# Kernel optimization log

Hardware: AMD Instinct MI355X
Metric: run time of the kernel (lower is better)

Reference implementation:

```python
import jax, jax.numpy as jnp
import numpy as np

N = 50000      # nodes
E = 800000     # edges (avg degree 16)
F_IN = 3       # dataset.num_node_features
H = 256        # hidden_channels
G = 64         # batch_size (num graphs)
OUT = 24       # lin_out output dim


def setup_inputs() -> dict:
    key = jax.random.key(0)
    ks = jax.random.split(key, 16)
    s = 0.05
    inp = {
        "x": jax.random.normal(ks[0], (N, F_IN), jnp.float32),
        "edge_index": jax.random.randint(ks[1], (2, E), 0, N, dtype=jnp.int32),
        "batch": jnp.sort(jax.random.randint(ks[2], (N,), 0, G, dtype=jnp.int32)),
        # layer 1 (F_IN -> H)
        "w_rel1": jax.random.normal(ks[3], (F_IN, H), jnp.float32) * s,
        "w_root1": jax.random.normal(ks[4], (F_IN, H), jnp.float32) * s,
        "b1": jnp.zeros((H,), jnp.float32),
        # layers 2..7 (H -> H), stacked
        "w_rel": jax.random.normal(ks[5], (6, H, H), jnp.float32) * s,
        "w_root": jax.random.normal(ks[6], (6, H, H), jnp.float32) * s,
        "b": jnp.zeros((6, H), jnp.float32),
        # output head
        "w_out": jax.random.normal(ks[7], (H, OUT), jnp.float32) * s,
        "b_out": jnp.zeros((OUT,), jnp.float32),
    }
    return inp


def reference(x, edge_index, batch, w_rel1, w_root1, b1, w_rel, w_root, b, w_out, b_out):
    src, dst = edge_index[0], edge_index[1]

    def conv(h, wr, wro, bb):
        # PyG GraphConv with add aggregation:
        # out_i = W_rel @ sum_{j -> i} h_j + b + W_root @ h_i
        agg = jax.ops.segment_sum(h[src], dst, num_segments=N)
        return agg @ wr + h @ wro + bb

    h = jax.nn.relu(conv(x, w_rel1, w_root1, b1))
    for i in range(6):
        h = jax.nn.relu(conv(h, w_rel[i], w_root[i], b[i]))

    # global_mean_pool over batch segment ids
    counts = jax.ops.segment_sum(jnp.ones((N,), h.dtype), batch, num_segments=G)
    pooled = jax.ops.segment_sum(h, batch, num_segments=G) / jnp.maximum(counts, 1.0)[:, None]

    # dropout is identity in eval mode
    return pooled @ w_out + b_out
```

## Files before the change

### kernel.cpp

```cpp
#include <hip/hip_runtime.h>

#define N_NODES 50000
#define MPAD 50048
#define N_EDGES 800000
#define H 256
#define K_CAT 512
#define G_BATCH 64
#define OUT_DIM 24

#define SCAN_BLK 256
#define NBLK ((N_NODES + SCAN_BLK - 1) / SCAN_BLK)

typedef __attribute__((ext_vector_type(8))) short short8;
typedef __attribute__((ext_vector_type(4))) float float4v;

__device__ __forceinline__ float bf2f(unsigned short u) {
    return __uint_as_float(((unsigned)u) << 16);
}
__device__ __forceinline__ unsigned short f2bf(float f) {
    unsigned x = __float_as_uint(f);
    unsigned r = (x + 0x7FFFu + ((x >> 16) & 1u)) >> 16;
    return (unsigned short)r;
}

__device__ __forceinline__ void async_copy16(void* lds, const void* g) {
    __builtin_amdgcn_global_load_lds(
        (const __attribute__((address_space(1))) unsigned int*)g,
        (__attribute__((address_space(3))) unsigned int*)lds, 16, 0, 0);
}



__global__ void histo_kernel(const int* __restrict__ dst, int* __restrict__ deg,
                             int* __restrict__ epos) {
    int e = blockIdx.x * blockDim.x + threadIdx.x;
    if (e < N_EDGES) epos[e] = atomicAdd(&deg[dst[e]], 1);
}

__global__ void scan_block(const int* __restrict__ deg, int* __restrict__ rowptr,
                           int* __restrict__ blockSums) {
    __shared__ int s[SCAN_BLK];
    int idx = blockIdx.x * SCAN_BLK + threadIdx.x;
    int v = (idx < N_NODES) ? deg[idx] : 0;
    s[threadIdx.x] = v;
    __syncthreads();
    for (int off = 1; off < SCAN_BLK; off <<= 1) {
        int t = (threadIdx.x >= off) ? s[threadIdx.x - off] : 0;
        __syncthreads();
        s[threadIdx.x] += t;
        __syncthreads();
    }
    if (idx < N_NODES) rowptr[idx] = s[threadIdx.x] - v;
    if (threadIdx.x == SCAN_BLK - 1) blockSums[blockIdx.x] = s[threadIdx.x];
}

__global__ void scan_finish(int* __restrict__ rowptr, const int* __restrict__ blockSums) {
    __shared__ int s[SCAN_BLK];
    int t = threadIdx.x;
    int v = (t < NBLK) ? blockSums[t] : 0;
    s[t] = v;
    __syncthreads();
    for (int off = 1; off < SCAN_BLK; off <<= 1) {
        int tv = (t >= off) ? s[t - off] : 0;
        __syncthreads();
        s[t] += tv;
        __syncthreads();
    }
    int prefix = (blockIdx.x > 0) ? s[blockIdx.x - 1] : 0;
    int idx = blockIdx.x * SCAN_BLK + t;
    if (idx < N_NODES) rowptr[idx] += prefix;
    if (blockIdx.x == 0 && t == 0) rowptr[N_NODES] = s[NBLK - 1];
}

__global__ void fill_csr(const int* __restrict__ src, const int* __restrict__ dst,
                         const int* __restrict__ rowptr, const int* __restrict__ epos,
                         int* __restrict__ csr_src) {
    int e = blockIdx.x * blockDim.x + threadIdx.x;
    if (e >= N_EDGES) return;
    csr_src[rowptr[dst[e]] + epos[e]] = src[e];
}


__global__ void prep_weights(const float* __restrict__ w_rel, const float* __restrict__ w_root,
                             unsigned short* __restrict__ WcatT) {
    int idx = blockIdx.x * blockDim.x + threadIdx.x;
    if (idx >= 6 * K_CAT * H) return;
    int n = idx & (H - 1);
    int k = (idx >> 8) & (K_CAT - 1);
    int l = idx >> 17;
    float v;
    if (k < H) {
        int f = (k & 0xC0) | ((k & 3) << 4) | ((k >> 2) & 15);
        v = w_rel[(size_t)l * H * H + f * H + n];
    } else {
        v = w_root[(size_t)l * H * H + (k - H) * H + n];
    }
    WcatT[(size_t)l * H * K_CAT + (size_t)n * K_CAT + k] = f2bf(v);
}


__global__ void agg3(const float* __restrict__ x, const int* __restrict__ rowptr,
                     const int* __restrict__ csr_src, float* __restrict__ agg) {
    int n = blockIdx.x * blockDim.x + threadIdx.x;
    if (n >= N_NODES) return;
    int beg = rowptr[n], end = rowptr[n + 1];
    float a0 = 0.f, a1 = 0.f, a2 = 0.f;
    for (int i = beg; i < end; ++i) {
        int s = csr_src[i];
        a0 += x[s * 3 + 0];
        a1 += x[s * 3 + 1];
        a2 += x[s * 3 + 2];
    }
    agg[n * 3 + 0] = a0;
    agg[n * 3 + 1] = a1;
    agg[n * 3 + 2] = a2;
}

__global__ void layer1_kernel(const float* __restrict__ x, const float* __restrict__ agg,
                              const float* __restrict__ wr, const float* __restrict__ wro,
                              const float* __restrict__ bias, unsigned short* __restrict__ cat,
                              unsigned char* __restrict__ h8, float* __restrict__ hscale) {
    __shared__ unsigned char tmp[H];
    int n = blockIdx.x;
    int f = threadIdx.x;
    float a0 = agg[n * 3 + 0], a1 = agg[n * 3 + 1], a2 = agg[n * 3 + 2];
    float x0 = x[n * 3 + 0], x1 = x[n * 3 + 1], x2 = x[n * 3 + 2];
    float v = bias[f];
    v += a0 * wr[0 * H + f] + a1 * wr[1 * H + f] + a2 * wr[2 * H + f];
    v += x0 * wro[0 * H + f] + x1 * wro[1 * H + f] + x2 * wro[2 * H + f];
    v = fmaxf(v, 0.f);
    cat[(size_t)n * K_CAT + H + f] = f2bf(v);
    float m = v;
#pragma unroll
    for (int off = 1; off < 64; off <<= 1) m = fmaxf(m, __shfl_xor(m, off, 64));
    float inv = m > 0.f ? 255.f / m : 0.f;
    tmp[(f & 0xC0) | ((f & 15) << 2) | ((f >> 4) & 3)] = (unsigned char)(v * inv + 0.5f);
    if ((f & 63) == 0) hscale[n * 4 + (f >> 6)] = m * (1.f / 255.f);
    __syncthreads();
    if (f < 64) *(unsigned*)(h8 + (size_t)n * H + f * 4) = *(const unsigned*)(tmp + f * 4);
}


__global__ __launch_bounds__(256) void aggH(unsigned short* __restrict__ cat,
                                            const unsigned char* __restrict__ h8,
                                            const float* __restrict__ hscale,
                                            const int* __restrict__ rowptr,
                                            const int* __restrict__ csr_src) {
    int gtid = blockIdx.x * blockDim.x + threadIdx.x;
    int node = gtid >> 6;
    if (node >= N_NODES) return;
    int lane = threadIdx.x & 63;
    int sub = lane >> 4;
    int fl = lane & 15;
    int g = fl >> 2;
    int beg = rowptr[node], end = rowptr[node + 1];

    if (beg >= end) {
        if (sub == 0) {
            uint4 z = make_uint4(0, 0, 0, 0);
            unsigned short* o = cat + (size_t)node * K_CAT + fl * 16;
            *(uint4*)o = z;
            *(uint4*)(o + 8) = z;
        }
        return;
    }

    float acc[16] = {};
    const unsigned char* base = h8 + fl * 16;
    int last = end - 1;

    int ia = beg + sub;
    int ca = ia < end ? ia : last;
    int sa = csr_src[ca];
    int ib = beg + 4 + sub;
    int cb = ib < end ? ib : last;
    int sb = csr_src[cb];
    float sca = (ia < end) ? hscale[sa * 4 + g] : 0.f;
    uint4 qa = *(const uint4*)(base + (size_t)sa * H);

    for (int i = beg; i < end; i += 4) {
        int ic = i + 8 + sub;
        int cc = ic < end ? ic : last;
        int sn = csr_src[cc];
        int inb = i + 4 + sub;
        float scb = (inb < end) ? hscale[sb * 4 + g] : 0.f;
        uint4 qb = *(const uint4*)(base + (size_t)sb * H);

        float sc = sca;
        acc[0]  = fmaf((float)(qa.x & 0xffu), sc, acc[0]);
        acc[1]  = fmaf((float)((qa.x >> 8) & 0xffu), sc, acc[1]);
        acc[2]  = fmaf((float)((qa.x >> 16) & 0xffu), sc, acc[2]);
        acc[3]  = fmaf((float)(qa.x >> 24), sc, acc[3]);
        acc[4]  = fmaf((float)(qa.y & 0xffu), sc, acc[4]);
        acc[5]  = fmaf((float)((qa.y >> 8) & 0xffu), sc, acc[5]);
        acc[6]  = fmaf((float)((qa.y >> 16) & 0xffu), sc, acc[6]);
        acc[7]  = fmaf((float)(qa.y >> 24), sc, acc[7]);
        acc[8]  = fmaf((float)(qa.z & 0xffu), sc, acc[8]);
        acc[9]  = fmaf((float)((qa.z >> 8) & 0xffu), sc, acc[9]);
        acc[10] = fmaf((float)((qa.z >> 16) & 0xffu), sc, acc[10]);
        acc[11] = fmaf((float)(qa.z >> 24), sc, acc[11]);
        acc[12] = fmaf((float)(qa.w & 0xffu), sc, acc[12]);
        acc[13] = fmaf((float)((qa.w >> 8) & 0xffu), sc, acc[13]);
        acc[14] = fmaf((float)((qa.w >> 16) & 0xffu), sc, acc[14]);
        acc[15] = fmaf((float)(qa.w >> 24), sc, acc[15]);

        sa = sb; sb = sn; sca = scb; qa = qb;
    }

#pragma unroll
    for (int j = 0; j < 16; j++) {
        acc[j] += __shfl_xor(acc[j], 16, 64);
        acc[j] += __shfl_xor(acc[j], 32, 64);
    }

    if (sub == 0) {
        unsigned short* o = cat + (size_t)node * K_CAT + fl * 16;
        uint4 p0, p1;
        p0.x = (unsigned)f2bf(acc[0])  | ((unsigned)f2bf(acc[1]) << 16);
        p0.y = (unsigned)f2bf(acc[2])  | ((unsigned)f2bf(acc[3]) << 16);
        p0.z = (unsigned)f2bf(acc[4])  | ((unsigned)f2bf(acc[5]) << 16);
        p0.w = (unsigned)f2bf(acc[6])  | ((unsigned)f2bf(acc[7]) << 16);
        p1.x = (unsigned)f2bf(acc[8])  | ((unsigned)f2bf(acc[9]) << 16);
        p1.y = (unsigned)f2bf(acc[10]) | ((unsigned)f2bf(acc[11]) << 16);
        p1.z = (unsigned)f2bf(acc[12]) | ((unsigned)f2bf(acc[13]) << 16);
        p1.w = (unsigned)f2bf(acc[14]) | ((unsigned)f2bf(acc[15]) << 16);
        *(uint4*)o = p0;
        *(uint4*)(o + 8) = p1;
    }
}


#define GBM 128
#define GBN 128
#define GBK 64

__global__ __launch_bounds__(256) void gemm_mfma(
    const unsigned short* __restrict__ cat, const unsigned short* __restrict__ WcatT,
    const float* __restrict__ bias, unsigned short* __restrict__ catOut,
    unsigned char* __restrict__ h8, float* __restrict__ hscale) {
    __shared__ unsigned short sA[GBM][GBK];
    __shared__ unsigned short sB[GBN][GBK];

    const int tid = threadIdx.x;
    const int wave = tid >> 6;
    const int lane = tid & 63;
    const int quad = lane >> 4;
    const int l16 = lane & 15;
    const int wm0 = (wave & 1) * 64;
    const int wn0 = (wave >> 1) * 64;
    const int m0 = blockIdx.x * GBM;
    const int n0 = blockIdx.y * GBN;

    const int rowoff = lane >> 3;
    const int schunk = ((lane & 7) ^ rowoff) * 8;
    const unsigned short* Asrc[4];
    const unsigned short* Bsrc[4];
#pragma unroll
    for (int j = 0; j < 4; j++) {
        int q = wave * 4 + j;
        Asrc[j] = cat + (size_t)(m0 + q * 8 + rowoff) * K_CAT + schunk;
        Bsrc[j] = WcatT + (size_t)(n0 + q * 8 + rowoff) * K_CAT + schunk;
    }

    const int sw = l16 & 7;
    const int ca0 = (quad ^ sw) * 8;
    const int ca1 = ((4 + quad) ^ sw) * 8;

    float4v acc[4][4] = {};

    for (int kk = 0; kk < K_CAT; kk += GBK) {
#pragma unroll
        for (int j = 0; j < 4; j++) {
            char* da = (char*)sA + (wave * 4 + j) * 1024;
            char* db = (char*)sB + (wave * 4 + j) * 1024;
            async_copy16(da, Asrc[j] + kk);
            async_copy16(db, Bsrc[j] + kk);
        }
        __syncthreads();

        short8 a[4][2], b[4][2];
#pragma unroll
        for (int i = 0; i < 4; i++) {
            const unsigned short* ra = &sA[wm0 + i * 16 + l16][0];
            const unsigned short* rb = &sB[wn0 + i * 16 + l16][0];
            a[i][0] = *(const short8*)(ra + ca0);
            a[i][1] = *(const short8*)(ra + ca1);
            b[i][0] = *(const short8*)(rb + ca0);
            b[i][1] = *(const short8*)(rb + ca1);
        }
#pragma unroll
        for (int sub = 0; sub < 2; sub++)
#pragma unroll
            for (int mi = 0; mi < 4; mi++)
#pragma unroll
                for (int ni = 0; ni < 4; ni++)
                    acc[mi][ni] = __builtin_amdgcn_mfma_f32_16x16x32_bf16(
                        a[mi][sub], b[ni][sub], acc[mi][ni], 0, 0, 0);
        __syncthreads();
    }

    const int hb = n0 + wn0 + l16 * 4;
    const int gsc = (n0 + wn0) >> 6;
    float bcol[4];
#pragma unroll
    for (int ni = 0; ni < 4; ni++) bcol[ni] = bias[n0 + wn0 + ni * 16 + l16];

#pragma unroll
    for (int mi = 0; mi < 4; mi++) {
        int rowb = m0 + wm0 + mi * 16 + quad * 4;
#pragma unroll
        for (int r = 0; r < 4; r++) {
            int row = rowb + r;
            float v0 = fmaxf(acc[mi][0][r] + bcol[0], 0.f);
            float v1 = fmaxf(acc[mi][1][r] + bcol[1], 0.f);
            float v2 = fmaxf(acc[mi][2][r] + bcol[2], 0.f);
            float v3 = fmaxf(acc[mi][3][r] + bcol[3], 0.f);
            unsigned short* co = catOut + (size_t)row * K_CAT + H + n0 + wn0 + l16;
            co[0]  = f2bf(v0);
            co[16] = f2bf(v1);
            co[32] = f2bf(v2);
            co[48] = f2bf(v3);
            float m = fmaxf(fmaxf(v0, v1), fmaxf(v2, v3));
            m = fmaxf(m, __shfl_xor(m, 1, 64));
            m = fmaxf(m, __shfl_xor(m, 2, 64));
            m = fmaxf(m, __shfl_xor(m, 4, 64));
            m = fmaxf(m, __shfl_xor(m, 8, 64));
            float inv = m > 0.f ? 255.f / m : 0.f;
            unsigned p = (unsigned)(v0 * inv + 0.5f)
                       | ((unsigned)(v1 * inv + 0.5f) << 8)
                       | ((unsigned)(v2 * inv + 0.5f) << 16)
                       | ((unsigned)(v3 * inv + 0.5f) << 24);
            *(unsigned*)(h8 + (size_t)row * H + hb) = p;
            if (l16 == 0) hscale[row * 4 + gsc] = m * (1.f / 255.f);
        }
    }
}


__device__ __forceinline__ int lowerBound(const int* __restrict__ batch, int val) {
    int lo = 0, hi = N_NODES;
    while (lo < hi) {
        int mid = (lo + hi) >> 1;
        if (batch[mid] < val) lo = mid + 1; else hi = mid;
    }
    return lo;
}

__global__ void pool_partial(const unsigned short* __restrict__ cat, const int* __restrict__ batch,
                             float* __restrict__ pooled) {
    int g = blockIdx.x;
    int seg = blockIdx.y;
    int f = threadIdx.x;
    int start = lowerBound(batch, g);
    int end = lowerBound(batch, g + 1);
    int len = end - start;
    int s0 = start + (int)((long long)len * seg / 8);
    int s1 = start + (int)((long long)len * (seg + 1) / 8);
    float sum = 0.f;
    for (int n = s0; n < s1; ++n)
        sum += bf2f(cat[(size_t)n * K_CAT + H + f]);
    if (s1 > s0)
        atomicAdd(&pooled[g * H + f], sum);
}

__global__ void head_kernel(const float* __restrict__ pooled, const int* __restrict__ batch,
                            const float* __restrict__ w_out, const float* __restrict__ b_out,
                            float* __restrict__ out) {
    int g = blockIdx.x;
    int o = threadIdx.x;
    int start = lowerBound(batch, g);
    int end = lowerBound(batch, g + 1);
    float cnt = fmaxf((float)(end - start), 1.f);
    float sum = 0.f;
    for (int f = 0; f < H; ++f)
        sum += pooled[g * H + f] * w_out[f * OUT_DIM + o];
    out[g * OUT_DIM + o] = b_out[o] + sum / cnt;
}


extern "C" void kernel_launch(void* const* d_in, const int* in_sizes, int n_in,
                              void* d_out, int out_size, void* d_ws, size_t ws_size,
                              hipStream_t stream) {
    const float* x      = (const float*)d_in[0];
    const int*   ei     = (const int*)d_in[1];
    const int*   batch  = (const int*)d_in[2];
    const float* w_rel1 = (const float*)d_in[3];
    const float* w_root1= (const float*)d_in[4];
    const float* b1     = (const float*)d_in[5];
    const float* w_rel  = (const float*)d_in[6];
    const float* w_root = (const float*)d_in[7];
    const float* b      = (const float*)d_in[8];
    const float* w_out  = (const float*)d_in[9];
    const float* b_out  = (const float*)d_in[10];
    float* out = (float*)d_out;

    const int* src = ei;
    const int* dst = ei + N_EDGES;

    unsigned short* catA  = (unsigned short*)d_ws;
    unsigned short* catB  = catA + (size_t)MPAD * K_CAT;
    unsigned short* WcatT = catB + (size_t)MPAD * K_CAT;
    float* agg3buf = (float*)(WcatT + (size_t)6 * H * K_CAT);
    float* pooled  = agg3buf + (size_t)N_NODES * 4;
    float* hscale  = pooled + G_BATCH * H;
    int* rowptr    = (int*)(hscale + (size_t)MPAD * 4);
    int* degcur    = rowptr + (N_NODES + 1);
    int* blockSums = degcur + N_NODES;
    int* csr_src   = blockSums + SCAN_BLK;
    int* epos      = csr_src + N_EDGES;
    unsigned char* h8 = (unsigned char*)(epos + N_EDGES);

    hipMemsetAsync(degcur, 0, N_NODES * sizeof(int), stream);
    histo_kernel<<<(N_EDGES + 255) / 256, 256, 0, stream>>>(dst, degcur, epos);
    scan_block<<<NBLK, SCAN_BLK, 0, stream>>>(degcur, rowptr, blockSums);
    scan_finish<<<NBLK, SCAN_BLK, 0, stream>>>(rowptr, blockSums);
    fill_csr<<<(N_EDGES + 255) / 256, 256, 0, stream>>>(src, dst, rowptr, epos, csr_src);

    prep_weights<<<(6 * K_CAT * H + 255) / 256, 256, 0, stream>>>(w_rel, w_root, WcatT);

    agg3<<<(N_NODES + 255) / 256, 256, 0, stream>>>(x, rowptr, csr_src, agg3buf);
    layer1_kernel<<<N_NODES, H, 0, stream>>>(x, agg3buf, w_rel1, w_root1, b1, catA, h8, hscale);

    unsigned short* cur = catA;
    unsigned short* nxt = catB;
    for (int l = 0; l < 6; ++l) {
        aggH<<<(N_NODES * 64 + 255) / 256, 256, 0, stream>>>(cur, h8, hscale, rowptr, csr_src);
        dim3 grid(MPAD / GBM, H / GBN);
        gemm_mfma<<<grid, 256, 0, stream>>>(cur, WcatT + (size_t)l * H * K_CAT,
                                            b + (size_t)l * H, nxt, h8, hscale);
        unsigned short* t = cur; cur = nxt; nxt = t;
    }

    hipMemsetAsync(pooled, 0, G_BATCH * H * sizeof(float), stream);
    pool_partial<<<dim3(G_BATCH, 8), 256, 0, stream>>>(cur, batch, pooled);
    head_kernel<<<G_BATCH, OUT_DIM, 0, stream>>>(pooled, batch, w_out, b_out, out);
}
```

Measured before the change: 680.0 us.

## Switch u8 quantization to per-column scales and aggregate with packed integer adds

Replaces per-node, per-64-group u8 scales with per-feature-column max scales. The column maxima are gathered with atomicMax in the GEMM epilogue, and a separate quant_u8 pass writes h8. Because the scale no longer varies per node, aggH can sum raw u8 bytes with packed SIMD integer adds into 16-bit lanes and apply the scale once at the end. This removes the per-edge scale load and the float FMAs. It adds an extra quantize pass per layer, a colmax pass after layer 1, and a permuted feature layout applied to the weights and the head. A per-column scale may lose precision for nodes whose values are much smaller than the column maximum.

```diff
diff --git a/kernel.cpp b/kernel.cpp
--- a/kernel.cpp
+++ b/kernel.cpp
@@ -14,21 +14,21 @@
 typedef __attribute__((ext_vector_type(8))) short short8;
 typedef __attribute__((ext_vector_type(4))) float float4v;
 
-__device__ __forceinline__ float bf2f(unsigned short u) {
-    return __uint_as_float(((unsigned)u) << 16);
-}
+
 __device__ __forceinline__ unsigned short f2bf(float f) {
     unsigned x = __float_as_uint(f);
     unsigned r = (x + 0x7FFFu + ((x >> 16) & 1u)) >> 16;
     return (unsigned short)r;
 }
+__device__ __forceinline__ float bf2f(unsigned short u) {
+    return __uint_as_float(((unsigned)u) << 16);
+}
 
 __device__ __forceinline__ void async_copy16(void* lds, const void* g) {
     __builtin_amdgcn_global_load_lds(
         (const __attribute__((address_space(1))) unsigned int*)g,
         (__attribute__((address_space(3))) unsigned int*)lds, 16, 0, 0);
 }
-
 
 
 __global__ void histo_kernel(const int* __restrict__ dst, int* __restrict__ deg,
@@ -93,7 +93,9 @@
         int f = (k & 0xC0) | ((k & 3) << 4) | ((k >> 2) & 15);
         v = w_rel[(size_t)l * H * H + f * H + n];
     } else {
-        v = w_root[(size_t)l * H * H + (k - H) * H + n];
+        int kk = k - H;
+        int f = (kk & 0xC0) | ((kk & 3) << 4) | ((kk >> 2) & 15);
+        v = w_root[(size_t)l * H * H + f * H + n];
     }
     WcatT[(size_t)l * H * K_CAT + (size_t)n * K_CAT + k] = f2bf(v);
 }
@@ -118,9 +120,7 @@
 
 __global__ void layer1_kernel(const float* __restrict__ x, const float* __restrict__ agg,
                               const float* __restrict__ wr, const float* __restrict__ wro,
-                              const float* __restrict__ bias, unsigned short* __restrict__ cat,
-                              unsigned char* __restrict__ h8, float* __restrict__ hscale) {
-    __shared__ unsigned char tmp[H];
+                              const float* __restrict__ bias, unsigned short* __restrict__ cat) {
     int n = blockIdx.x;
     int f = threadIdx.x;
     float a0 = agg[n * 3 + 0], a1 = agg[n * 3 + 1], a2 = agg[n * 3 + 2];
@@ -128,22 +128,57 @@
     float v = bias[f];
     v += a0 * wr[0 * H + f] + a1 * wr[1 * H + f] + a2 * wr[2 * H + f];
     v += x0 * wro[0 * H + f] + x1 * wro[1 * H + f] + x2 * wro[2 * H + f];
-    v = fmaxf(v, 0.f);
-    cat[(size_t)n * K_CAT + H + f] = f2bf(v);
-    float m = v;
-#pragma unroll
-    for (int off = 1; off < 64; off <<= 1) m = fmaxf(m, __shfl_xor(m, off, 64));
-    float inv = m > 0.f ? 255.f / m : 0.f;
-    tmp[(f & 0xC0) | ((f & 15) << 2) | ((f >> 4) & 3)] = (unsigned char)(v * inv + 0.5f);
-    if ((f & 63) == 0) hscale[n * 4 + (f >> 6)] = m * (1.f / 255.f);
+    int bpos = (f & 0xC0) | ((f & 15) << 2) | ((f >> 4) & 3);
+    cat[(size_t)n * K_CAT + H + bpos] = f2bf(fmaxf(v, 0.f));
+}
+
+
+__global__ __launch_bounds__(256) void colmax_h(const unsigned short* __restrict__ cat,
+                                                float* __restrict__ cs) {
+    int wave = threadIdx.x >> 6, lane = threadIdx.x & 63;
+    int r0 = blockIdx.x * 512 + wave * 128;
+    float m0 = 0.f, m1 = 0.f, m2 = 0.f, m3 = 0.f;
+    for (int i = 0; i < 128; i++) {
+        int r = r0 + i;
+        if (r >= N_NODES) break;
+        uint2 v = *(const uint2*)(cat + (size_t)r * K_CAT + H + lane * 4);
+        m0 = fmaxf(m0, __uint_as_float(v.x << 16));
+        m1 = fmaxf(m1, __uint_as_float(v.x & 0xffff0000u));
+        m2 = fmaxf(m2, __uint_as_float(v.y << 16));
+        m3 = fmaxf(m3, __uint_as_float(v.y & 0xffff0000u));
+    }
+    atomicMax((unsigned*)&cs[lane * 4 + 0], __float_as_uint(m0));
+    atomicMax((unsigned*)&cs[lane * 4 + 1], __float_as_uint(m1));
+    atomicMax((unsigned*)&cs[lane * 4 + 2], __float_as_uint(m2));
+    atomicMax((unsigned*)&cs[lane * 4 + 3], __float_as_uint(m3));
+}
+
+
+__global__ __launch_bounds__(256) void quant_u8(const unsigned short* __restrict__ cat,
+                                                const float* __restrict__ cs,
+                                                unsigned char* __restrict__ h8) {
+    __shared__ float inv[H];
+    int t = threadIdx.x;
+    float c = cs[t];
+    inv[t] = c > 0.f ? 255.f / c : 0.f;
     __syncthreads();
-    if (f < 64) *(unsigned*)(h8 + (size_t)n * H + f * 4) = *(const unsigned*)(tmp + f * 4);
+    int node = blockIdx.x * 4 + (t >> 6);
+    if (node >= N_NODES) return;
+    int s4 = (t & 63) * 4;
+    uint2 v = *(const uint2*)(cat + (size_t)node * K_CAT + H + s4);
+    float f0 = __uint_as_float(v.x << 16), f1 = __uint_as_float(v.x & 0xffff0000u);
+    float f2 = __uint_as_float(v.y << 16), f3 = __uint_as_float(v.y & 0xffff0000u);
+    unsigned q = (unsigned)(f0 * inv[s4] + 0.5f)
+               | ((unsigned)(f1 * inv[s4 + 1] + 0.5f) << 8)
+               | ((unsigned)(f2 * inv[s4 + 2] + 0.5f) << 16)
+               | ((unsigned)(f3 * inv[s4 + 3] + 0.5f) << 24);
+    *(unsigned*)(h8 + (size_t)node * H + s4) = q;
 }
 
 
 __global__ __launch_bounds__(256) void aggH(unsigned short* __restrict__ cat,
                                             const unsigned char* __restrict__ h8,
-                                            const float* __restrict__ hscale,
+                                            const float* __restrict__ cs,
                                             const int* __restrict__ rowptr,
                                             const int* __restrict__ csr_src) {
     int gtid = blockIdx.x * blockDim.x + threadIdx.x;
@@ -152,81 +187,75 @@
     int lane = threadIdx.x & 63;
     int sub = lane >> 4;
     int fl = lane & 15;
-    int g = fl >> 2;
     int beg = rowptr[node], end = rowptr[node + 1];
+    unsigned short* o = cat + (size_t)node * K_CAT + fl * 16;
 
     if (beg >= end) {
         if (sub == 0) {
             uint4 z = make_uint4(0, 0, 0, 0);
-            unsigned short* o = cat + (size_t)node * K_CAT + fl * 16;
             *(uint4*)o = z;
             *(uint4*)(o + 8) = z;
         }
         return;
     }
 
-    float acc[16] = {};
+    unsigned accE[4] = {0, 0, 0, 0}, accO[4] = {0, 0, 0, 0};
     const unsigned char* base = h8 + fl * 16;
     int last = end - 1;
 
-    int ia = beg + sub;
-    int ca = ia < end ? ia : last;
-    int sa = csr_src[ca];
-    int ib = beg + 4 + sub;
-    int cb = ib < end ? ib : last;
-    int sb = csr_src[cb];
-    float sca = (ia < end) ? hscale[sa * 4 + g] : 0.f;
-    uint4 qa = *(const uint4*)(base + (size_t)sa * H);
-
-    for (int i = beg; i < end; i += 4) {
-        int ic = i + 8 + sub;
-        int cc = ic < end ? ic : last;
-        int sn = csr_src[cc];
-        int inb = i + 4 + sub;
-        float scb = (inb < end) ? hscale[sb * 4 + g] : 0.f;
-        uint4 qb = *(const uint4*)(base + (size_t)sb * H);
-
-        float sc = sca;
-        acc[0]  = fmaf((float)(qa.x & 0xffu), sc, acc[0]);
-        acc[1]  = fmaf((float)((qa.x >> 8) & 0xffu), sc, acc[1]);
-        acc[2]  = fmaf((float)((qa.x >> 16) & 0xffu), sc, acc[2]);
-        acc[3]  = fmaf((float)(qa.x >> 24), sc, acc[3]);
-        acc[4]  = fmaf((float)(qa.y & 0xffu), sc, acc[4]);
-        acc[5]  = fmaf((float)((qa.y >> 8) & 0xffu), sc, acc[5]);
-        acc[6]  = fmaf((float)((qa.y >> 16) & 0xffu), sc, acc[6]);
-        acc[7]  = fmaf((float)(qa.y >> 24), sc, acc[7]);
-        acc[8]  = fmaf((float)(qa.z & 0xffu), sc, acc[8]);
-        acc[9]  = fmaf((float)((qa.z >> 8) & 0xffu), sc, acc[9]);
-        acc[10] = fmaf((float)((qa.z >> 16) & 0xffu), sc, acc[10]);
-        acc[11] = fmaf((float)(qa.z >> 24), sc, acc[11]);
-        acc[12] = fmaf((float)(qa.w & 0xffu), sc, acc[12]);
-        acc[13] = fmaf((float)((qa.w >> 8) & 0xffu), sc, acc[13]);
-        acc[14] = fmaf((float)((qa.w >> 16) & 0xffu), sc, acc[14]);
-        acc[15] = fmaf((float)(qa.w >> 24), sc, acc[15]);
-
-        sa = sb; sb = sn; sca = scb; qa = qb;
-    }
-
-#pragma unroll
-    for (int j = 0; j < 16; j++) {
-        acc[j] += __shfl_xor(acc[j], 16, 64);
-        acc[j] += __shfl_xor(acc[j], 32, 64);
-    }
-
-    if (sub == 0) {
-        unsigned short* o = cat + (size_t)node * K_CAT + fl * 16;
-        uint4 p0, p1;
-        p0.x = (unsigned)f2bf(acc[0])  | ((unsigned)f2bf(acc[1]) << 16);
-        p0.y = (unsigned)f2bf(acc[2])  | ((unsigned)f2bf(acc[3]) << 16);
-        p0.z = (unsigned)f2bf(acc[4])  | ((unsigned)f2bf(acc[5]) << 16);
-        p0.w = (unsigned)f2bf(acc[6])  | ((unsigned)f2bf(acc[7]) << 16);
-        p1.x = (unsigned)f2bf(acc[8])  | ((unsigned)f2bf(acc[9]) << 16);
-        p1.y = (unsigned)f2bf(acc[10]) | ((unsigned)f2bf(acc[11]) << 16);
-        p1.z = (unsigned)f2bf(acc[12]) | ((unsigned)f2bf(acc[13]) << 16);
-        p1.w = (unsigned)f2bf(acc[14]) | ((unsigned)f2bf(acc[15]) << 16);
-        *(uint4*)o = p0;
-        *(uint4*)(o + 8) = p1;
-    }
+    for (int i0 = beg; i0 < end; i0 += 4) {
+        int idx = i0 + sub;
+        int s = csr_src[idx < end ? idx : last];
+        uint4 q = *(const uint4*)(base + (size_t)s * H);
+        if (idx >= end) { q.x = 0u; q.y = 0u; q.z = 0u; q.w = 0u; }
+        accE[0] += q.x & 0x00FF00FFu;  accO[0] += (q.x >> 8) & 0x00FF00FFu;
+        accE[1] += q.y & 0x00FF00FFu;  accO[1] += (q.y >> 8) & 0x00FF00FFu;
+        accE[2] += q.z & 0x00FF00FFu;  accO[2] += (q.z >> 8) & 0x00FF00FFu;
+        accE[3] += q.w & 0x00FF00FFu;  accO[3] += (q.w >> 8) & 0x00FF00FFu;
+    }
+
+#pragma unroll
+    for (int j = 0; j < 4; j++) {
+        accE[j] += __shfl_xor(accE[j], 16, 64);
+        accE[j] += __shfl_xor(accE[j], 32, 64);
+        accO[j] += __shfl_xor(accO[j], 16, 64);
+        accO[j] += __shfl_xor(accO[j], 32, 64);
+    }
+    if (sub != 0) return;
+
+    const float k = 1.f / 255.f;
+    float4 c0 = *(const float4*)(cs + fl * 16);
+    float4 c1 = *(const float4*)(cs + fl * 16 + 4);
+    float4 c2 = *(const float4*)(cs + fl * 16 + 8);
+    float4 c3 = *(const float4*)(cs + fl * 16 + 12);
+    float v0  = (float)(accE[0] & 0xFFFFu) * (c0.x * k);
+    float v1  = (float)(accO[0] & 0xFFFFu) * (c0.y * k);
+    float v2  = (float)(accE[0] >> 16)     * (c0.z * k);
+    float v3  = (float)(accO[0] >> 16)     * (c0.w * k);
+    float v4  = (float)(accE[1] & 0xFFFFu) * (c1.x * k);
+    float v5  = (float)(accO[1] & 0xFFFFu) * (c1.y * k);
+    float v6  = (float)(accE[1] >> 16)     * (c1.z * k);
+    float v7  = (float)(accO[1] >> 16)     * (c1.w * k);
+    float v8  = (float)(accE[2] & 0xFFFFu) * (c2.x * k);
+    float v9  = (float)(accO[2] & 0xFFFFu) * (c2.y * k);
+    float v10 = (float)(accE[2] >> 16)     * (c2.z * k);
+    float v11 = (float)(accO[2] >> 16)     * (c2.w * k);
+    float v12 = (float)(accE[3] & 0xFFFFu) * (c3.x * k);
+    float v13 = (float)(accO[3] & 0xFFFFu) * (c3.y * k);
+    float v14 = (float)(accE[3] >> 16)     * (c3.z * k);
+    float v15 = (float)(accO[3] >> 16)     * (c3.w * k);
+
+    uint4 p0, p1;
+    p0.x = (unsigned)f2bf(v0)  | ((unsigned)f2bf(v1) << 16);
+    p0.y = (unsigned)f2bf(v2)  | ((unsigned)f2bf(v3) << 16);
+    p0.z = (unsigned)f2bf(v4)  | ((unsigned)f2bf(v5) << 16);
+    p0.w = (unsigned)f2bf(v6)  | ((unsigned)f2bf(v7) << 16);
+    p1.x = (unsigned)f2bf(v8)  | ((unsigned)f2bf(v9) << 16);
+    p1.y = (unsigned)f2bf(v10) | ((unsigned)f2bf(v11) << 16);
+    p1.z = (unsigned)f2bf(v12) | ((unsigned)f2bf(v13) << 16);
+    p1.w = (unsigned)f2bf(v14) | ((unsigned)f2bf(v15) << 16);
+    *(uint4*)o = p0;
+    *(uint4*)(o + 8) = p1;
 }
 
 
@@ -237,7 +266,7 @@
 __global__ __launch_bounds__(256) void gemm_mfma(
     const unsigned short* __restrict__ cat, const unsigned short* __restrict__ WcatT,
     const float* __restrict__ bias, unsigned short* __restrict__ catOut,
-    unsigned char* __restrict__ h8, float* __restrict__ hscale) {
+    float* __restrict__ csNext) {
     __shared__ unsigned short sA[GBM][GBK];
     __shared__ unsigned short sB[GBN][GBK];
 
@@ -299,11 +328,11 @@
         __syncthreads();
     }
 
-    const int hb = n0 + wn0 + l16 * 4;
-    const int gsc = (n0 + wn0) >> 6;
+    const int colbase = n0 + wn0;
     float bcol[4];
 #pragma unroll
-    for (int ni = 0; ni < 4; ni++) bcol[ni] = bias[n0 + wn0 + ni * 16 + l16];
+    for (int ni = 0; ni < 4; ni++) bcol[ni] = bias[colbase + ni * 16 + l16];
+    float cm[4] = {0.f, 0.f, 0.f, 0.f};
 
 #pragma unroll
     for (int mi = 0; mi < 4; mi++) {
@@ -315,24 +344,26 @@
             float v1 = fmaxf(acc[mi][1][r] + bcol[1], 0.f);
             float v2 = fmaxf(acc[mi][2][r] + bcol[2], 0.f);
             float v3 = fmaxf(acc[mi][3][r] + bcol[3], 0.f);
-            unsigned short* co = catOut + (size_t)row * K_CAT + H + n0 + wn0 + l16;
-            co[0]  = f2bf(v0);
-            co[16] = f2bf(v1);
-            co[32] = f2bf(v2);
-            co[48] = f2bf(v3);
-            float m = fmaxf(fmaxf(v0, v1), fmaxf(v2, v3));
-            m = fmaxf(m, __shfl_xor(m, 1, 64));
-            m = fmaxf(m, __shfl_xor(m, 2, 64));
-            m = fmaxf(m, __shfl_xor(m, 4, 64));
-            m = fmaxf(m, __shfl_xor(m, 8, 64));
-            float inv = m > 0.f ? 255.f / m : 0.f;
-            unsigned p = (unsigned)(v0 * inv + 0.5f)
-                       | ((unsigned)(v1 * inv + 0.5f) << 8)
-                       | ((unsigned)(v2 * inv + 0.5f) << 16)
-                       | ((unsigned)(v3 * inv + 0.5f) << 24);
-            *(unsigned*)(h8 + (size_t)row * H + hb) = p;
-            if (l16 == 0) hscale[row * 4 + gsc] = m * (1.f / 255.f);
+            uint2 p;
+            p.x = (unsigned)f2bf(v0) | ((unsigned)f2bf(v1) << 16);
+            p.y = (unsigned)f2bf(v2) | ((unsigned)f2bf(v3) << 16);
+            *(uint2*)(catOut + (size_t)row * K_CAT + H + colbase + l16 * 4) = p;
+            bool val = row < N_NODES;
+            cm[0] = fmaxf(cm[0], val ? v0 : 0.f);
+            cm[1] = fmaxf(cm[1], val ? v1 : 0.f);
+            cm[2] = fmaxf(cm[2], val ? v2 : 0.f);
+            cm[3] = fmaxf(cm[3], val ? v3 : 0.f);
         }
+    }
+#pragma unroll
+    for (int ni = 0; ni < 4; ni++) {
+        cm[ni] = fmaxf(cm[ni], __shfl_xor(cm[ni], 16, 64));
+        cm[ni] = fmaxf(cm[ni], __shfl_xor(cm[ni], 32, 64));
+    }
+    if (quad == 0) {
+#pragma unroll
+        for (int ni = 0; ni < 4; ni++)
+            atomicMax((unsigned*)&csNext[colbase + l16 * 4 + ni], __float_as_uint(cm[ni]));
     }
 }
 
@@ -372,8 +403,10 @@
     int end = lowerBound(batch, g + 1);
     float cnt = fmaxf((float)(end - start), 1.f);
     float sum = 0.f;
-    for (int f = 0; f < H; ++f)
-        sum += pooled[g * H + f] * w_out[f * OUT_DIM + o];
+    for (int b = 0; b < H; ++b) {
+        int f = (b & 0xC0) | ((b & 3) << 4) | ((b >> 2) & 15);
+        sum += pooled[g * H + b] * w_out[f * OUT_DIM + o];
+    }
     out[g * OUT_DIM + o] = b_out[o] + sum / cnt;
 }
 
@@ -402,15 +435,16 @@
     unsigned short* WcatT = catB + (size_t)MPAD * K_CAT;
     float* agg3buf = (float*)(WcatT + (size_t)6 * H * K_CAT);
     float* pooled  = agg3buf + (size_t)N_NODES * 4;
-    float* hscale  = pooled + G_BATCH * H;
-    int* rowptr    = (int*)(hscale + (size_t)MPAD * 4);
+    float* csAll   = pooled + G_BATCH * H;
+    unsigned char* h8 = (unsigned char*)(csAll + 8 * H);
+    int* rowptr    = (int*)(h8 + (size_t)N_NODES * H);
     int* degcur    = rowptr + (N_NODES + 1);
     int* blockSums = degcur + N_NODES;
     int* csr_src   = blockSums + SCAN_BLK;
     int* epos      = csr_src + N_EDGES;
-    unsigned char* h8 = (unsigned char*)(epos + N_EDGES);
 
     hipMemsetAsync(degcur, 0, N_NODES * sizeof(int), stream);
+    hipMemsetAsync(csAll, 0, 8 * H * sizeof(float), stream);
     histo_kernel<<<(N_EDGES + 255) / 256, 256, 0, stream>>>(dst, degcur, epos);
     scan_block<<<NBLK, SCAN_BLK, 0, stream>>>(degcur, rowptr, blockSums);
     scan_finish<<<NBLK, SCAN_BLK, 0, stream>>>(rowptr, blockSums);
@@ -419,15 +453,19 @@
     prep_weights<<<(6 * K_CAT * H + 255) / 256, 256, 0, stream>>>(w_rel, w_root, WcatT);
 
     agg3<<<(N_NODES + 255) / 256, 256, 0, stream>>>(x, rowptr, csr_src, agg3buf);
-    layer1_kernel<<<N_NODES, H, 0, stream>>>(x, agg3buf, w_rel1, w_root1, b1, catA, h8, hscale);
+    layer1_kernel<<<N_NODES, H, 0, stream>>>(x, agg3buf, w_rel1, w_root1, b1, catA);
+    colmax_h<<<(N_NODES + 511) / 512, 256, 0, stream>>>(catA, csAll + 1 * H);
 
     unsigned short* cur = catA;
     unsigned short* nxt = catB;
-    for (int l = 0; l < 6; ++l) {
-        aggH<<<(N_NODES * 64 + 255) / 256, 256, 0, stream>>>(cur, h8, hscale, rowptr, csr_src);
+    for (int l = 1; l <= 6; ++l) {
+        quant_u8<<<(N_NODES + 3) / 4, 256, 0, stream>>>(cur, csAll + (size_t)l * H, h8);
+        aggH<<<(N_NODES * 64 + 255) / 256, 256, 0, stream>>>(cur, h8, csAll + (size_t)l * H,
+                                                             rowptr, csr_src);
         dim3 grid(MPAD / GBM, H / GBN);
-        gemm_mfma<<<grid, 256, 0, stream>>>(cur, WcatT + (size_t)l * H * K_CAT,
-                                            b + (size_t)l * H, nxt, h8, hscale);
+        gemm_mfma<<<grid, 256, 0, stream>>>(cur, WcatT + (size_t)(l - 1) * H * K_CAT,
+                                            b + (size_t)(l - 1) * H, nxt,
+                                            csAll + (size_t)(l + 1) * H);
         unsigned short* t = cur; cur = nxt; nxt = t;
     }
 
```

New measurement: 1.234 ms. 81.4% more time.
